# Optimization experiments

Measured on AMD Instinct MI355X. Metric: run time of the kernel, lower is better.

Reference implementation:

```python
import jax, jax.numpy as jnp
import numpy as np

EMB = 192
HEADS = 6
WIN = (8, 8)
N = WIN[0] * WIN[1]  # 64
B_ = 2048
NW = 1024  # mask windows per image; B_ % NW == 0


def _relative_position_index():
    coords_h = np.arange(WIN[0])
    coords_w = np.arange(WIN[1])
    coords = np.stack(np.meshgrid(coords_h, coords_w, indexing='ij'))  # (2,Wh,Ww)
    cf = coords.reshape(2, -1)
    rel = cf[:, :, None] - cf[:, None, :]  # (2,N,N)
    rel = rel.transpose(1, 2, 0)
    rel[:, :, 0] += WIN[0] - 1
    rel[:, :, 1] += WIN[1] - 1
    rel[:, :, 0] *= 2 * WIN[1] - 1
    return rel.sum(-1).astype(np.int32)  # (N,N)


def setup_inputs() -> dict:
    key = jax.random.key(0)
    ks = jax.random.split(key, 12)
    num_bias = (2 * WIN[0] - 1) * (2 * WIN[1] - 1)  # 225
    s = 0.02
    return {
        'q': jax.random.normal(ks[0], (B_, N, EMB), jnp.float32),
        'k': jax.random.normal(ks[1], (B_, N, EMB), jnp.float32),
        'v': jax.random.normal(ks[2], (B_, N, EMB), jnp.float32),
        'mask': jax.random.normal(ks[3], (NW, N, N), jnp.float32),
        'Wq': jax.random.normal(ks[4], (EMB, EMB), jnp.float32) * s,
        'bq': jnp.zeros((EMB,), jnp.float32),
        'Wk': jax.random.normal(ks[5], (EMB, EMB), jnp.float32) * s,
        'bk': jnp.zeros((EMB,), jnp.float32),
        'Wv': jax.random.normal(ks[6], (EMB, EMB), jnp.float32) * s,
        'bv': jnp.zeros((EMB,), jnp.float32),
        'Wp': jax.random.normal(ks[7], (EMB, EMB), jnp.float32) * s,
        'bp': jnp.zeros((EMB,), jnp.float32),
        'bias_table': jax.random.normal(ks[8], (num_bias, HEADS), jnp.float32) * s,
        'rel_index': jnp.asarray(_relative_position_index()),
    }


def reference(q, k, v, mask, Wq, bq, Wk, bk, Wv, bv, Wp, bp, bias_table, rel_index):
    head_dim = EMB // HEADS
    scale = head_dim ** -0.5

    def split_heads(x):
        # (B_,N,C) -> (B_,H,N,D)
        return x.reshape(B_, N, HEADS, head_dim).transpose(0, 2, 1, 3)

    qh = split_heads(q @ Wq + bq) * scale
    kh = split_heads(k @ Wk + bk)
    vh = split_heads(v @ Wv + bv)

    attn = jnp.einsum('bhnd,bhmd->bhnm', qh, kh)  # (B_,H,N,N)

    # gathered relative position bias: (N,N,H) -> (H,N,N)
    rel_bias = bias_table[rel_index.reshape(-1)].reshape(N, N, HEADS).transpose(2, 0, 1)
    attn = attn + rel_bias[None]

    # mask add: reshape to (B, nW, H, N, N) and broadcast mask over batch/heads
    nW = mask.shape[0]
    attn = attn.reshape(-1, nW, HEADS, N, N) + mask[None, :, None]
    attn = attn.reshape(-1, HEADS, N, N)
    attn = jax.nn.softmax(attn, axis=-1)

    x = jnp.einsum('bhnm,bhmd->bhnd', attn, vh)  # (B_,H,N,D)
    x = x.transpose(0, 2, 1, 3).reshape(B_, N, EMB)
    x = x @ Wp + bp
    return (x, attn)
```

## Files before the change

### kernel.cpp

```cpp
#include <hip/hip_runtime.h>
#include <hip/hip_bf16.h>

typedef __attribute__((ext_vector_type(8))) short   bf16x8;
typedef __attribute__((ext_vector_type(4))) float   f32x4;
typedef __attribute__((ext_vector_type(4))) unsigned short u16x4;
typedef unsigned short u16;

#define NTOK 64
#define CEMB 192
#define NH   6
#define ROWB 384
#define VROWB 128

__device__ __forceinline__ u16 f2b(float f) {
  unsigned u = __float_as_uint(f);
  unsigned r = (u + 0x7fffu + ((u >> 16) & 1u)) >> 16;
  return (u16)r;
}

__device__ __forceinline__ int swz(int row, int colbyte) {
  return colbyte ^ ((((row >> 3) ^ row) & 7) << 4);
}

__global__ void prep_kernel(const float* __restrict__ Wq, const float* __restrict__ Wk,
                            const float* __restrict__ Wv, const float* __restrict__ Wp,
                            const float* __restrict__ btab, const int* __restrict__ ridx,
                            u16* __restrict__ WT, float* __restrict__ rb) {
  int idx = blockIdx.x * 256 + threadIdx.x;
  if (idx < 4 * 36864) {
    int m = idx / 36864;
    int e = idx - m * 36864;
    int n = e / CEMB;
    int k = e - n * CEMB;
    const float* W = (m == 0) ? Wq : (m == 1) ? Wk : (m == 2) ? Wv : Wp;
    WT[idx] = f2b(W[k * CEMB + n]);
  } else {
    int i2 = idx - 4 * 36864;
    if (i2 < NH * 4096) {
      int h = i2 >> 12;
      int ij = i2 & 4095;
      rb[i2] = btab[ridx[ij] * NH + h];
    }
  }
}

__global__ __launch_bounds__(512, 4)
void wattn_kernel(const float* __restrict__ qg, const float* __restrict__ kg,
                  const float* __restrict__ vg, const float* __restrict__ maskg,
                  const float* __restrict__ bq, const float* __restrict__ bk,
                  const float* __restrict__ bv, const float* __restrict__ bp,
                  const u16* __restrict__ WT, const float* __restrict__ rb,
                  float* __restrict__ xout, float* __restrict__ attn_out) {
  __shared__ __align__(16) char smem[81920];
  char* sQ = smem;
  char* sK = smem + 24576;
  char* sV = smem + 49152;
  const int tid  = threadIdx.x;
  const int wave = tid >> 6;
  const int lane = tid & 63;
  const int l15  = lane & 15;
  const int lhi  = lane >> 4;
  char* sP = smem + 73728 + wave * 1024;
  const int b    = blockIdx.x;
  const float scale = 0.17677669529663687f;

  {
    const size_t base = (size_t)b * NTOK * CEMB;
    #pragma unroll
    for (int m = 0; m < 3; ++m) {
      const float* src = (m == 0 ? qg : m == 1 ? kg : vg) + base;
      char* dst = (m == 0 ? sQ : m == 1 ? sK : sV);
      #pragma unroll
      for (int it = 0; it < 6; ++it) {
        int fi  = it * 512 + tid;
        int row = fi / 48;
        int ce  = (fi - row * 48) * 4;
        const float4 v4 = reinterpret_cast<const float4*>(src)[fi];
        u16x4 p;
        p.x = f2b(v4.x); p.y = f2b(v4.y); p.z = f2b(v4.z); p.w = f2b(v4.w);
        *reinterpret_cast<u16x4*>(dst + row * ROWB + swz(row, ce * 2)) = p;
      }
    }
  }
  __syncthreads();

  f32x4 accv[5][4];
  #pragma unroll
  for (int si = 0; si < 5; ++si) {
    int strip = wave + si * 8;
    if (strip < 36) {
      int m  = strip / 12;
      int ct = strip - m * 12;
      const char* Xs = (m == 0) ? sQ : (m == 1) ? sK : sV;
      const u16* Wt = WT + m * 36864 + (ct * 16 + l15) * CEMB + lhi * 8;
      f32x4 z = {0.f, 0.f, 0.f, 0.f};
      #pragma unroll
      for (int rt = 0; rt < 4; ++rt) accv[si][rt] = z;
      #pragma unroll
      for (int ks = 0; ks < 6; ++ks) {
        bf16x8 bw = *reinterpret_cast<const bf16x8*>(Wt + ks * 32);
        #pragma unroll
        for (int rt = 0; rt < 4; ++rt) {
          int row = rt * 16 + l15;
          bf16x8 ax = *reinterpret_cast<const bf16x8*>(Xs + row * ROWB + swz(row, ks * 64 + lhi * 16));
          accv[si][rt] = __builtin_amdgcn_mfma_f32_16x16x32_bf16(ax, bw, accv[si][rt], 0, 0, 0);
        }
      }
    }
  }
  __syncthreads();

  #pragma unroll
  for (int si = 0; si < 5; ++si) {
    int strip = wave + si * 8;
    if (strip < 36) {
      int m  = strip / 12;
      int ct = strip - m * 12;
      int n  = ct * 16 + l15;
      float bval = ((m == 0) ? bq : (m == 1) ? bk : bv)[n];
      if (m == 0) {
        #pragma unroll
        for (int rt = 0; rt < 4; ++rt)
          #pragma unroll
          for (int r = 0; r < 4; ++r) {
            int row = rt * 16 + lhi * 4 + r;
            *reinterpret_cast<u16*>(sQ + row * ROWB + swz(row, n * 2)) = f2b((accv[si][rt][r] + bval) * scale);
          }
      } else if (m == 1) {
        #pragma unroll
        for (int rt = 0; rt < 4; ++rt)
          #pragma unroll
          for (int r = 0; r < 4; ++r) {
            int row = rt * 16 + lhi * 4 + r;
            *reinterpret_cast<u16*>(sK + row * ROWB + swz(row, n * 2)) = f2b(accv[si][rt][r] + bval);
          }
      } else {
        #pragma unroll
        for (int rt = 0; rt < 4; ++rt) {
          int t0 = rt * 16 + lhi * 4;
          u16x4 pk;
          #pragma unroll
          for (int r = 0; r < 4; ++r) pk[r] = f2b(accv[si][rt][r] + bval);
          *reinterpret_cast<u16x4*>(sV + n * VROWB + swz(n, t0 * 2)) = pk;
        }
      }
    }
  }
  __syncthreads();

  const float* maskw = maskg + (size_t)(b & 1023) * 4096;
  #pragma unroll
  for (int ui = 0; ui < 3; ++ui) {
    int u  = wave + ui * 8;
    int h  = u >> 2;
    int rt = u & 3;
    int irow = rt * 16 + lhi * 4;

    const float* rbp = rb + h * 4096 + irow * 64 + l15;
    const float* mkp = maskw + irow * 64 + l15;
    float rbv[4][4], mkv[4][4];
    #pragma unroll
    for (int ct = 0; ct < 4; ++ct)
      #pragma unroll
      for (int r = 0; r < 4; ++r) {
        rbv[ct][r] = rbp[r * 64 + ct * 16];
        mkv[ct][r] = mkp[r * 64 + ct * 16];
      }

    int qrow = rt * 16 + l15;
    bf16x8 aq = *reinterpret_cast<const bf16x8*>(sQ + qrow * ROWB + swz(qrow, h * 64 + lhi * 16));
    f32x4 sv[4];
    #pragma unroll
    for (int ct = 0; ct < 4; ++ct) {
      int krow = ct * 16 + l15;
      bf16x8 bkf = *reinterpret_cast<const bf16x8*>(sK + krow * ROWB + swz(krow, h * 64 + lhi * 16));
      f32x4 z = {0.f, 0.f, 0.f, 0.f};
      sv[ct] = __builtin_amdgcn_mfma_f32_16x16x32_bf16(aq, bkf, z, 0, 0, 0);
    }

    float lg[4][4];
    #pragma unroll
    for (int ct = 0; ct < 4; ++ct)
      #pragma unroll
      for (int r = 0; r < 4; ++r)
        lg[ct][r] = sv[ct][r] + rbv[ct][r] + mkv[ct][r];

    float pr[4][4];
    #pragma unroll
    for (int r = 0; r < 4; ++r) {
      float mx = fmaxf(fmaxf(lg[0][r], lg[1][r]), fmaxf(lg[2][r], lg[3][r]));
      mx = fmaxf(mx, __shfl_xor(mx, 1));
      mx = fmaxf(mx, __shfl_xor(mx, 2));
      mx = fmaxf(mx, __shfl_xor(mx, 4));
      mx = fmaxf(mx, __shfl_xor(mx, 8));
      float e0 = __expf(lg[0][r] - mx), e1 = __expf(lg[1][r] - mx);
      float e2 = __expf(lg[2][r] - mx), e3 = __expf(lg[3][r] - mx);
      float sum = e0 + e1 + e2 + e3;
      sum += __shfl_xor(sum, 1);
      sum += __shfl_xor(sum, 2);
      sum += __shfl_xor(sum, 4);
      sum += __shfl_xor(sum, 8);
      float inv = 1.0f / sum;
      pr[0][r] = e0 * inv; pr[1][r] = e1 * inv; pr[2][r] = e2 * inv; pr[3][r] = e3 * inv;
    }

    float* ap = attn_out + (((size_t)b * NH + h) * NTOK + irow) * NTOK;
    #pragma unroll
    for (int ct = 0; ct < 4; ++ct)
      #pragma unroll
      for (int r = 0; r < 4; ++r)
        ap[r * 64 + ct * 16 + l15] = pr[ct][r];

    f32x4 xa[2];
    { f32x4 z = {0.f, 0.f, 0.f, 0.f}; xa[0] = z; xa[1] = z; }
    #pragma unroll
    for (int ks = 0; ks < 2; ++ks) {
      #pragma unroll
      for (int c = 0; c < 2; ++c)
        #pragma unroll
        for (int r = 0; r < 4; ++r) {
          int col  = c * 16 + l15;
          int kg   = col >> 3;
          int j    = col & 7;
          int prow = lhi * 4 + r;
          *reinterpret_cast<u16*>(sP + ((kg * 16 + prow) * 8 + j) * 2) = f2b(pr[ks * 2 + c][r]);
        }
      bf16x8 apf = *reinterpret_cast<const bf16x8*>(sP + lane * 16);
      #pragma unroll
      for (int ctv = 0; ctv < 2; ++ctv) {
        int vrow = h * 32 + ctv * 16 + l15;
        bf16x8 bvf = *reinterpret_cast<const bf16x8*>(sV + vrow * VROWB + swz(vrow, ks * 64 + lhi * 16));
        xa[ctv] = __builtin_amdgcn_mfma_f32_16x16x32_bf16(apf, bvf, xa[ctv], 0, 0, 0);
      }
    }

    #pragma unroll
    for (int ctv = 0; ctv < 2; ++ctv)
      #pragma unroll
      for (int r = 0; r < 4; ++r) {
        int xrow = rt * 16 + lhi * 4 + r;
        int xcol = h * 32 + ctv * 16 + l15;
        *reinterpret_cast<u16*>(sQ + xrow * ROWB + swz(xrow, xcol * 2)) = f2b(xa[ctv][r]);
      }
  }
  __syncthreads();

  #pragma unroll
  for (int ui = 0; ui < 3; ++ui) {
    int u2 = wave + ui * 8;
    int ct = u2 % 12;
    int rh = u2 / 12;
    const u16* Wt = WT + 3 * 36864 + (ct * 16 + l15) * CEMB + lhi * 8;
    f32x4 oa[2];
    { f32x4 z = {0.f, 0.f, 0.f, 0.f}; oa[0] = z; oa[1] = z; }
    #pragma unroll
    for (int ks = 0; ks < 6; ++ks) {
      bf16x8 bw = *reinterpret_cast<const bf16x8*>(Wt + ks * 32);
      #pragma unroll
      for (int rr = 0; rr < 2; ++rr) {
        int xrow = rh * 32 + rr * 16 + l15;
        bf16x8 ax = *reinterpret_cast<const bf16x8*>(sQ + xrow * ROWB + swz(xrow, ks * 64 + lhi * 16));
        oa[rr] = __builtin_amdgcn_mfma_f32_16x16x32_bf16(ax, bw, oa[rr], 0, 0, 0);
      }
    }
    float bias = bp[ct * 16 + l15];
    #pragma unroll
    for (int rr = 0; rr < 2; ++rr)
      #pragma unroll
      for (int r = 0; r < 4; ++r)
        xout[((size_t)b * NTOK + rh * 32 + rr * 16 + lhi * 4 + r) * CEMB + ct * 16 + l15] = oa[rr][r] + bias;
  }
}

extern "C" void kernel_launch(void* const* d_in, const int* in_sizes, int n_in,
                              void* d_out, int out_size, void* d_ws, size_t ws_size,
                              hipStream_t stream) {
  const float* q    = (const float*)d_in[0];
  const float* k    = (const float*)d_in[1];
  const float* v    = (const float*)d_in[2];
  const float* mask = (const float*)d_in[3];
  const float* Wq   = (const float*)d_in[4];
  const float* bq   = (const float*)d_in[5];
  const float* Wk   = (const float*)d_in[6];
  const float* bk   = (const float*)d_in[7];
  const float* Wv   = (const float*)d_in[8];
  const float* bv   = (const float*)d_in[9];
  const float* Wp   = (const float*)d_in[10];
  const float* bp   = (const float*)d_in[11];
  const float* btab = (const float*)d_in[12];
  const int*   ridx = (const int*)d_in[13];

  u16*   WT = (u16*)d_ws;
  float* rb = (float*)((char*)d_ws + 4 * 36864 * 2);

  float* xout = (float*)d_out;
  float* attn = xout + (size_t)2048 * NTOK * CEMB;

  prep_kernel<<<672, 256, 0, stream>>>(Wq, Wk, Wv, Wp, btab, ridx, WT, rb);
  wattn_kernel<<<2048, 512, 0, stream>>>(q, k, v, mask, bq, bk, bv, bp, WT, rb, xout, attn);
}
```

Measured before the change: 221.4 us.

## Split fused window attention into projection and attention kernels via output scratch

Measured after the change: 760.9 us. +243.6%, slower.

```diff
diff --git a/kernel.cpp b/kernel.cpp
--- a/kernel.cpp
+++ b/kernel.cpp
@@ -3,19 +3,23 @@
 
 typedef __attribute__((ext_vector_type(8))) short   bf16x8;
 typedef __attribute__((ext_vector_type(4))) float   f32x4;
-typedef __attribute__((ext_vector_type(4))) unsigned short u16x4;
 typedef unsigned short u16;
 
 #define NTOK 64
 #define CEMB 192
 #define NH   6
 #define ROWB 384
-#define VROWB 128
 
 __device__ __forceinline__ u16 f2b(float f) {
   unsigned u = __float_as_uint(f);
   unsigned r = (u + 0x7fffu + ((u >> 16) & 1u)) >> 16;
   return (u16)r;
+}
+
+__device__ __forceinline__ unsigned cvtpk(float lo, float hi) {
+  unsigned r;
+  asm("v_cvt_pk_bf16_f32 %0, %1, %2" : "=v"(r) : "v"(lo), "v"(hi));
+  return r;
 }
 
 __device__ __forceinline__ int swz(int row, int colbyte) {
@@ -44,117 +48,109 @@
   }
 }
 
-__global__ __launch_bounds__(512, 4)
-void wattn_kernel(const float* __restrict__ qg, const float* __restrict__ kg,
-                  const float* __restrict__ vg, const float* __restrict__ maskg,
-                  const float* __restrict__ bq, const float* __restrict__ bk,
-                  const float* __restrict__ bv, const float* __restrict__ bp,
-                  const u16* __restrict__ WT, const float* __restrict__ rb,
-                  float* __restrict__ xout, float* __restrict__ attn_out) {
-  __shared__ __align__(16) char smem[81920];
-  char* sQ = smem;
-  char* sK = smem + 24576;
-  char* sV = smem + 49152;
+__global__ __launch_bounds__(256, 6)
+void proj_kernel(const float* __restrict__ qg, const float* __restrict__ kg,
+                 const float* __restrict__ vg,
+                 const float* __restrict__ bq, const float* __restrict__ bk,
+                 const float* __restrict__ bv,
+                 const u16* __restrict__ WT,
+                 float* __restrict__ xout, float* __restrict__ attn_out) {
+  __shared__ __align__(16) char sT[24576];
   const int tid  = threadIdx.x;
   const int wave = tid >> 6;
   const int lane = tid & 63;
   const int l15  = lane & 15;
   const int lhi  = lane >> 4;
-  char* sP = smem + 73728 + wave * 1024;
-  const int b    = blockIdx.x;
-  const float scale = 0.17677669529663687f;
-
-  {
-    const size_t base = (size_t)b * NTOK * CEMB;
-    #pragma unroll
-    for (int m = 0; m < 3; ++m) {
-      const float* src = (m == 0 ? qg : m == 1 ? kg : vg) + base;
-      char* dst = (m == 0 ? sQ : m == 1 ? sK : sV);
-      #pragma unroll
-      for (int it = 0; it < 6; ++it) {
-        int fi  = it * 512 + tid;
-        int row = fi / 48;
-        int ce  = (fi - row * 48) * 4;
-        const float4 v4 = reinterpret_cast<const float4*>(src)[fi];
-        u16x4 p;
-        p.x = f2b(v4.x); p.y = f2b(v4.y); p.z = f2b(v4.z); p.w = f2b(v4.w);
-        *reinterpret_cast<u16x4*>(dst + row * ROWB + swz(row, ce * 2)) = p;
-      }
-    }
+  const int m = blockIdx.x / 2048;
+  const int b = blockIdx.x - m * 2048;
+
+  const float* src  = (m == 0 ? qg : m == 1 ? kg : vg) + (size_t)b * NTOK * CEMB;
+  const float* bias = (m == 0 ? bq : m == 1 ? bk : bv);
+
+  #pragma unroll
+  for (int it = 0; it < 12; ++it) {
+    int fi  = it * 256 + tid;
+    int row = fi / 48;
+    int ce  = (fi - row * 48) * 4;
+    const float4 v4 = reinterpret_cast<const float4*>(src)[fi];
+    uint2 w;
+    w.x = cvtpk(v4.x, v4.y);
+    w.y = cvtpk(v4.z, v4.w);
+    *reinterpret_cast<uint2*>(sT + row * ROWB + swz(row, ce * 2)) = w;
   }
   __syncthreads();
 
-  f32x4 accv[5][4];
-  #pragma unroll
-  for (int si = 0; si < 5; ++si) {
-    int strip = wave + si * 8;
-    if (strip < 36) {
-      int m  = strip / 12;
-      int ct = strip - m * 12;
-      const char* Xs = (m == 0) ? sQ : (m == 1) ? sK : sV;
-      const u16* Wt = WT + m * 36864 + (ct * 16 + l15) * CEMB + lhi * 8;
-      f32x4 z = {0.f, 0.f, 0.f, 0.f};
-      #pragma unroll
-      for (int rt = 0; rt < 4; ++rt) accv[si][rt] = z;
-      #pragma unroll
-      for (int ks = 0; ks < 6; ++ks) {
-        bf16x8 bw = *reinterpret_cast<const bf16x8*>(Wt + ks * 32);
+  u16* attnU = (u16*)(attn_out + (size_t)b * 24576 + 16384);
+  u16* xU    = (u16*)(xout + (size_t)b * 12288);
+  const float scale = (m == 0) ? 0.17677669529663687f : 1.0f;
+
+  #pragma unroll
+  for (int si = 0; si < 3; ++si) {
+    int ct = wave + si * 4;
+    const u16* Wt = WT + m * 36864 + (ct * 16 + l15) * CEMB + lhi * 8;
+    f32x4 acc[4];
+    { f32x4 z = {0.f, 0.f, 0.f, 0.f}; acc[0]=z; acc[1]=z; acc[2]=z; acc[3]=z; }
+    #pragma unroll
+    for (int ks = 0; ks < 6; ++ks) {
+      bf16x8 bw = *reinterpret_cast<const bf16x8*>(Wt + ks * 32);
+      #pragma unroll
+      for (int rt = 0; rt < 4; ++rt) {
+        int row = rt * 16 + l15;
+        bf16x8 ax = *reinterpret_cast<const bf16x8*>(sT + row * ROWB + swz(row, ks * 64 + lhi * 16));
+        acc[rt] = __builtin_amdgcn_mfma_f32_16x16x32_bf16(ax, bw, acc[rt], 0, 0, 0);
+      }
+    }
+    int c = ct * 16 + l15;
+    float bval = bias[c];
+    if (m == 2) {
+      #pragma unroll
+      for (int rt = 0; rt < 4; ++rt) {
+        int t0 = rt * 16 + lhi * 4;
+        uint2 w;
+        w.x = cvtpk(acc[rt][0] + bval, acc[rt][1] + bval);
+        w.y = cvtpk(acc[rt][2] + bval, acc[rt][3] + bval);
+        *reinterpret_cast<uint2*>(xU + 8192 + c * 64 + t0) = w;
+      }
+    } else {
+      int p = c >> 6;
+      u16* base = (p == 2 ? xU : attnU + p * 8192) + m * 4096 + (c & 63);
+      #pragma unroll
+      for (int rt = 0; rt < 4; ++rt)
         #pragma unroll
-        for (int rt = 0; rt < 4; ++rt) {
-          int row = rt * 16 + l15;
-          bf16x8 ax = *reinterpret_cast<const bf16x8*>(Xs + row * ROWB + swz(row, ks * 64 + lhi * 16));
-          accv[si][rt] = __builtin_amdgcn_mfma_f32_16x16x32_bf16(ax, bw, accv[si][rt], 0, 0, 0);
-        }
-      }
-    }
-  }
-  __syncthreads();
-
-  #pragma unroll
-  for (int si = 0; si < 5; ++si) {
-    int strip = wave + si * 8;
-    if (strip < 36) {
-      int m  = strip / 12;
-      int ct = strip - m * 12;
-      int n  = ct * 16 + l15;
-      float bval = ((m == 0) ? bq : (m == 1) ? bk : bv)[n];
-      if (m == 0) {
-        #pragma unroll
-        for (int rt = 0; rt < 4; ++rt)
-          #pragma unroll
-          for (int r = 0; r < 4; ++r) {
-            int row = rt * 16 + lhi * 4 + r;
-            *reinterpret_cast<u16*>(sQ + row * ROWB + swz(row, n * 2)) = f2b((accv[si][rt][r] + bval) * scale);
-          }
-      } else if (m == 1) {
-        #pragma unroll
-        for (int rt = 0; rt < 4; ++rt)
-          #pragma unroll
-          for (int r = 0; r < 4; ++r) {
-            int row = rt * 16 + lhi * 4 + r;
-            *reinterpret_cast<u16*>(sK + row * ROWB + swz(row, n * 2)) = f2b(accv[si][rt][r] + bval);
-          }
-      } else {
-        #pragma unroll
-        for (int rt = 0; rt < 4; ++rt) {
-          int t0 = rt * 16 + lhi * 4;
-          u16x4 pk;
-          #pragma unroll
-          for (int r = 0; r < 4; ++r) pk[r] = f2b(accv[si][rt][r] + bval);
-          *reinterpret_cast<u16x4*>(sV + n * VROWB + swz(n, t0 * 2)) = pk;
-        }
-      }
-    }
-  }
-  __syncthreads();
-
+        for (int r = 0; r < 4; ++r)
+          base[(rt * 16 + lhi * 4 + r) * 64] = f2b((acc[rt][r] + bval) * scale);
+    }
+  }
+}
+
+__global__ __launch_bounds__(512, 6)
+void attn_kernel(const float* __restrict__ maskg, const float* __restrict__ bp,
+                 const u16* __restrict__ WT, const float* __restrict__ rb,
+                 float* __restrict__ xout, float* __restrict__ attn_out) {
+  __shared__ __align__(16) char smem[32768];
+  char* sX = smem;
+  const int tid  = threadIdx.x;
+  const int wave = tid >> 6;
+  const int lane = tid & 63;
+  const int l15  = lane & 15;
+  const int lhi  = lane >> 4;
+  char* sP = smem + 24576 + wave * 1024;
+  const int b = blockIdx.x;
+
+  const u16* attnU = (const u16*)(attn_out + (size_t)b * 24576 + 16384);
+  const u16* xU    = (const u16*)(xout + (size_t)b * 12288);
   const float* maskw = maskg + (size_t)(b & 1023) * 4096;
+
+  const int rt   = wave & 3;
+  const int hq   = wave >> 2;
+  const int irow = rt * 16 + lhi * 4;
+
   #pragma unroll
   for (int ui = 0; ui < 3; ++ui) {
-    int u  = wave + ui * 8;
-    int h  = u >> 2;
-    int rt = u & 3;
-    int irow = rt * 16 + lhi * 4;
+    int h = 2 * ui + hq;
+    int p = h >> 1;
+    const u16* region = (p == 2) ? xU : attnU + p * 8192;
+    int cl = (h & 1) * 32 + lhi * 8;
 
     const float* rbp = rb + h * 4096 + irow * 64 + l15;
     const float* mkp = maskw + irow * 64 + l15;
@@ -167,13 +163,11 @@
         mkv[ct][r] = mkp[r * 64 + ct * 16];
       }
 
-    int qrow = rt * 16 + l15;
-    bf16x8 aq = *reinterpret_cast<const bf16x8*>(sQ + qrow * ROWB + swz(qrow, h * 64 + lhi * 16));
+    bf16x8 aq = *reinterpret_cast<const bf16x8*>(region + (rt * 16 + l15) * 64 + cl);
     f32x4 sv[4];
     #pragma unroll
     for (int ct = 0; ct < 4; ++ct) {
-      int krow = ct * 16 + l15;
-      bf16x8 bkf = *reinterpret_cast<const bf16x8*>(sK + krow * ROWB + swz(krow, h * 64 + lhi * 16));
+      bf16x8 bkf = *reinterpret_cast<const bf16x8*>(region + 4096 + (ct * 16 + l15) * 64 + cl);
       f32x4 z = {0.f, 0.f, 0.f, 0.f};
       sv[ct] = __builtin_amdgcn_mfma_f32_16x16x32_bf16(aq, bkf, z, 0, 0, 0);
     }
@@ -220,16 +214,16 @@
         #pragma unroll
         for (int r = 0; r < 4; ++r) {
           int col  = c * 16 + l15;
-          int kg   = col >> 3;
+          int kgp  = col >> 3;
           int j    = col & 7;
           int prow = lhi * 4 + r;
-          *reinterpret_cast<u16*>(sP + ((kg * 16 + prow) * 8 + j) * 2) = f2b(pr[ks * 2 + c][r]);
+          *reinterpret_cast<u16*>(sP + ((kgp * 16 + prow) * 8 + j) * 2) = f2b(pr[ks * 2 + c][r]);
         }
       bf16x8 apf = *reinterpret_cast<const bf16x8*>(sP + lane * 16);
       #pragma unroll
       for (int ctv = 0; ctv < 2; ++ctv) {
-        int vrow = h * 32 + ctv * 16 + l15;
-        bf16x8 bvf = *reinterpret_cast<const bf16x8*>(sV + vrow * VROWB + swz(vrow, ks * 64 + lhi * 16));
+        int chan = h * 32 + ctv * 16 + l15;
+        bf16x8 bvf = *reinterpret_cast<const bf16x8*>(xU + 8192 + chan * 64 + ks * 32 + lhi * 8);
         xa[ctv] = __builtin_amdgcn_mfma_f32_16x16x32_bf16(apf, bvf, xa[ctv], 0, 0, 0);
       }
     }
@@ -240,8 +234,10 @@
       for (int r = 0; r < 4; ++r) {
         int xrow = rt * 16 + lhi * 4 + r;
         int xcol = h * 32 + ctv * 16 + l15;
-        *reinterpret_cast<u16*>(sQ + xrow * ROWB + swz(xrow, xcol * 2)) = f2b(xa[ctv][r]);
-      }
+        *reinterpret_cast<u16*>(sX + xrow * ROWB + swz(xrow, xcol * 2)) = f2b(xa[ctv][r]);
+      }
+
+    if (ui == 1) __syncthreads();
   }
   __syncthreads();
 
@@ -259,7 +255,7 @@
       #pragma unroll
       for (int rr = 0; rr < 2; ++rr) {
         int xrow = rh * 32 + rr * 16 + l15;
-        bf16x8 ax = *reinterpret_cast<const bf16x8*>(sQ + xrow * ROWB + swz(xrow, ks * 64 + lhi * 16));
+        bf16x8 ax = *reinterpret_cast<const bf16x8*>(sX + xrow * ROWB + swz(xrow, ks * 64 + lhi * 16));
         oa[rr] = __builtin_amdgcn_mfma_f32_16x16x32_bf16(ax, bw, oa[rr], 0, 0, 0);
       }
     }
@@ -297,5 +293,6 @@
   float* attn = xout + (size_t)2048 * NTOK * CEMB;
 
   prep_kernel<<<672, 256, 0, stream>>>(Wq, Wk, Wv, Wp, btab, ridx, WT, rb);
-  wattn_kernel<<<2048, 512, 0, stream>>>(q, k, v, mask, bq, bk, bv, bp, WT, rb, xout, attn);
-}
+  proj_kernel<<<6144, 256, 0, stream>>>(q, k, v, bq, bk, bv, WT, xout, attn);
+  attn_kernel<<<2048, 512, 0, stream>>>(mask, bp, WT, rb, xout, attn);
+}
```

## Split QKV projection per matrix, hoist mask loads, use packed bf16 converts

Applied to the files above, without the earlier changes.

New measurement: 203.9 us. -7.9%, faster.

```diff
diff --git a/kernel.cpp b/kernel.cpp
--- a/kernel.cpp
+++ b/kernel.cpp
@@ -3,7 +3,6 @@
 
 typedef __attribute__((ext_vector_type(8))) short   bf16x8;
 typedef __attribute__((ext_vector_type(4))) float   f32x4;
-typedef __attribute__((ext_vector_type(4))) unsigned short u16x4;
 typedef unsigned short u16;
 
 #define NTOK 64
@@ -16,6 +15,12 @@
   unsigned u = __float_as_uint(f);
   unsigned r = (u + 0x7fffu + ((u >> 16) & 1u)) >> 16;
   return (u16)r;
+}
+
+__device__ __forceinline__ unsigned cvtpk(float lo, float hi) {
+  unsigned r;
+  asm("v_cvt_pk_bf16_f32 %0, %1, %2" : "=v"(r) : "v"(lo), "v"(hi));
+  return r;
 }
 
 __device__ __forceinline__ int swz(int row, int colbyte) {
@@ -61,7 +66,7 @@
   const int l15  = lane & 15;
   const int lhi  = lane >> 4;
   char* sP = smem + 73728 + wave * 1024;
-  const int b    = blockIdx.x;
+  const int b = blockIdx.x;
   const float scale = 0.17677669529663687f;
 
   {
@@ -76,96 +81,101 @@
         int row = fi / 48;
         int ce  = (fi - row * 48) * 4;
         const float4 v4 = reinterpret_cast<const float4*>(src)[fi];
-        u16x4 p;
-        p.x = f2b(v4.x); p.y = f2b(v4.y); p.z = f2b(v4.z); p.w = f2b(v4.w);
-        *reinterpret_cast<u16x4*>(dst + row * ROWB + swz(row, ce * 2)) = p;
+        uint2 w;
+        w.x = cvtpk(v4.x, v4.y);
+        w.y = cvtpk(v4.z, v4.w);
+        *reinterpret_cast<uint2*>(dst + row * ROWB + swz(row, ce * 2)) = w;
       }
     }
   }
   __syncthreads();
 
-  f32x4 accv[5][4];
   #pragma unroll
-  for (int si = 0; si < 5; ++si) {
-    int strip = wave + si * 8;
-    if (strip < 36) {
-      int m  = strip / 12;
-      int ct = strip - m * 12;
-      const char* Xs = (m == 0) ? sQ : (m == 1) ? sK : sV;
-      const u16* Wt = WT + m * 36864 + (ct * 16 + l15) * CEMB + lhi * 8;
-      f32x4 z = {0.f, 0.f, 0.f, 0.f};
-      #pragma unroll
-      for (int rt = 0; rt < 4; ++rt) accv[si][rt] = z;
-      #pragma unroll
-      for (int ks = 0; ks < 6; ++ks) {
-        bf16x8 bw = *reinterpret_cast<const bf16x8*>(Wt + ks * 32);
+  for (int m = 0; m < 3; ++m) {
+    const char* Xs = (m == 0) ? sQ : (m == 1) ? sK : sV;
+    const float* bias = (m == 0) ? bq : (m == 1) ? bk : bv;
+    f32x4 acc[2][4];
+    #pragma unroll
+    for (int si = 0; si < 2; ++si) {
+      int strip = wave + si * 8;
+      if (strip < 12) {
+        const u16* Wt = WT + m * 36864 + (strip * 16 + l15) * CEMB + lhi * 8;
         #pragma unroll
-        for (int rt = 0; rt < 4; ++rt) {
-          int row = rt * 16 + l15;
-          bf16x8 ax = *reinterpret_cast<const bf16x8*>(Xs + row * ROWB + swz(row, ks * 64 + lhi * 16));
-          accv[si][rt] = __builtin_amdgcn_mfma_f32_16x16x32_bf16(ax, bw, accv[si][rt], 0, 0, 0);
+        for (int rt = 0; rt < 4; ++rt) { f32x4 z = {0.f,0.f,0.f,0.f}; acc[si][rt] = z; }
+        #pragma unroll
+        for (int ks = 0; ks < 6; ++ks) {
+          bf16x8 bw = *reinterpret_cast<const bf16x8*>(Wt + ks * 32);
+          #pragma unroll
+          for (int rt = 0; rt < 4; ++rt) {
+            int row = rt * 16 + l15;
+            bf16x8 ax = *reinterpret_cast<const bf16x8*>(Xs + row * ROWB + swz(row, ks * 64 + lhi * 16));
+            acc[si][rt] = __builtin_amdgcn_mfma_f32_16x16x32_bf16(ax, bw, acc[si][rt], 0, 0, 0);
+          }
         }
       }
     }
+    __syncthreads();
+    #pragma unroll
+    for (int si = 0; si < 2; ++si) {
+      int strip = wave + si * 8;
+      if (strip < 12) {
+        int c = strip * 16 + l15;
+        float bval = bias[c];
+        if (m == 0) {
+          #pragma unroll
+          for (int rt = 0; rt < 4; ++rt)
+            #pragma unroll
+            for (int r = 0; r < 4; ++r) {
+              int row = rt * 16 + lhi * 4 + r;
+              *reinterpret_cast<u16*>(sQ + row * ROWB + swz(row, c * 2)) = f2b((acc[si][rt][r] + bval) * scale);
+            }
+        } else if (m == 1) {
+          #pragma unroll
+          for (int rt = 0; rt < 4; ++rt)
+            #pragma unroll
+            for (int r = 0; r < 4; ++r) {
+              int row = rt * 16 + lhi * 4 + r;
+              *reinterpret_cast<u16*>(sK + row * ROWB + swz(row, c * 2)) = f2b(acc[si][rt][r] + bval);
+            }
+        } else {
+          #pragma unroll
+          for (int rt = 0; rt < 4; ++rt) {
+            int t0 = rt * 16 + lhi * 4;
+            uint2 w;
+            w.x = cvtpk(acc[si][rt][0] + bval, acc[si][rt][1] + bval);
+            w.y = cvtpk(acc[si][rt][2] + bval, acc[si][rt][3] + bval);
+            *reinterpret_cast<uint2*>(sV + c * VROWB + swz(c, t0 * 2)) = w;
+          }
+        }
+      }
+    }
   }
   __syncthreads();
 
+  const float* maskw = maskg + (size_t)(b & 1023) * 4096;
+  const int rt   = wave & 3;
+  const int irow = rt * 16 + lhi * 4;
+
+  const float* mkp = maskw + irow * 64 + l15;
+  float mkv[4][4];
   #pragma unroll
-  for (int si = 0; si < 5; ++si) {
-    int strip = wave + si * 8;
-    if (strip < 36) {
-      int m  = strip / 12;
-      int ct = strip - m * 12;
-      int n  = ct * 16 + l15;
-      float bval = ((m == 0) ? bq : (m == 1) ? bk : bv)[n];
-      if (m == 0) {
-        #pragma unroll
-        for (int rt = 0; rt < 4; ++rt)
-          #pragma unroll
-          for (int r = 0; r < 4; ++r) {
-            int row = rt * 16 + lhi * 4 + r;
-            *reinterpret_cast<u16*>(sQ + row * ROWB + swz(row, n * 2)) = f2b((accv[si][rt][r] + bval) * scale);
-          }
-      } else if (m == 1) {
-        #pragma unroll
-        for (int rt = 0; rt < 4; ++rt)
-          #pragma unroll
-          for (int r = 0; r < 4; ++r) {
-            int row = rt * 16 + lhi * 4 + r;
-            *reinterpret_cast<u16*>(sK + row * ROWB + swz(row, n * 2)) = f2b(accv[si][rt][r] + bval);
-          }
-      } else {
-        #pragma unroll
-        for (int rt = 0; rt < 4; ++rt) {
-          int t0 = rt * 16 + lhi * 4;
-          u16x4 pk;
-          #pragma unroll
-          for (int r = 0; r < 4; ++r) pk[r] = f2b(accv[si][rt][r] + bval);
-          *reinterpret_cast<u16x4*>(sV + n * VROWB + swz(n, t0 * 2)) = pk;
-        }
-      }
-    }
-  }
-  __syncthreads();
-
-  const float* maskw = maskg + (size_t)(b & 1023) * 4096;
+  for (int ct = 0; ct < 4; ++ct)
+    #pragma unroll
+    for (int r = 0; r < 4; ++r)
+      mkv[ct][r] = mkp[r * 64 + ct * 16];
+
   #pragma unroll
   for (int ui = 0; ui < 3; ++ui) {
-    int u  = wave + ui * 8;
-    int h  = u >> 2;
-    int rt = u & 3;
-    int irow = rt * 16 + lhi * 4;
+    int u = wave + ui * 8;
+    int h = u >> 2;
 
     const float* rbp = rb + h * 4096 + irow * 64 + l15;
-    const float* mkp = maskw + irow * 64 + l15;
-    float rbv[4][4], mkv[4][4];
+    float rbv[4][4];
     #pragma unroll
     for (int ct = 0; ct < 4; ++ct)
       #pragma unroll
-      for (int r = 0; r < 4; ++r) {
+      for (int r = 0; r < 4; ++r)
         rbv[ct][r] = rbp[r * 64 + ct * 16];
-        mkv[ct][r] = mkp[r * 64 + ct * 16];
-      }
 
     int qrow = rt * 16 + l15;
     bf16x8 aq = *reinterpret_cast<const bf16x8*>(sQ + qrow * ROWB + swz(qrow, h * 64 + lhi * 16));
@@ -220,10 +230,10 @@
         #pragma unroll
         for (int r = 0; r < 4; ++r) {
           int col  = c * 16 + l15;
-          int kg   = col >> 3;
+          int kgp  = col >> 3;
           int j    = col & 7;
           int prow = lhi * 4 + r;
-          *reinterpret_cast<u16*>(sP + ((kg * 16 + prow) * 8 + j) * 2) = f2b(pr[ks * 2 + c][r]);
+          *reinterpret_cast<u16*>(sP + ((kgp * 16 + prow) * 8 + j) * 2) = f2b(pr[ks * 2 + c][r]);
         }
       bf16x8 apf = *reinterpret_cast<const bf16x8*>(sP + lane * 16);
       #pragma unroll
```
